# Kernel tuning notes

Hardware: AMD Instinct MI355X
Metric: run time of the kernel (lower is better)

Reference implementation:

```python
import jax, jax.numpy as jnp
import numpy as np

D_MODEL = 2048
N_HEADS = 16
D_HEAD = 128
N_GROUPS = 4          # KV heads = N_HEADS // N_GROUPS = 4
D_FF = 2048           # hard-coded default in FeedForward
EPS = 1e-6


def setup_inputs() -> dict:
    key = jax.random.key(0)
    ks = jax.random.split(key, 16)
    B, S = 4, 1024
    Hkv = N_HEADS // N_GROUPS
    s = 0.02
    inp = {
        "x": jax.random.normal(ks[0], (B, S, D_MODEL), jnp.float32),
        "scale1": jnp.ones((D_MODEL,), jnp.float32),
        "Wq": jax.random.normal(ks[1], (D_MODEL, N_HEADS * D_HEAD), jnp.float32) * s,
        "bq": jnp.zeros((N_HEADS * D_HEAD,), jnp.float32),
        "Wk": jax.random.normal(ks[2], (D_MODEL, Hkv * D_HEAD), jnp.float32) * s,
        "bk": jnp.zeros((Hkv * D_HEAD,), jnp.float32),
        "Wv": jax.random.normal(ks[3], (D_MODEL, Hkv * D_HEAD), jnp.float32) * s,
        "bv": jnp.zeros((Hkv * D_HEAD,), jnp.float32),
        "Wo": jax.random.normal(ks[4], (N_HEADS * D_HEAD, D_MODEL), jnp.float32) * s,
        "bo": jnp.zeros((D_MODEL,), jnp.float32),
        "W1": jax.random.normal(ks[5], (D_MODEL, D_FF), jnp.float32) * s,
        "b1": jnp.zeros((D_FF,), jnp.float32),
        "W2": jax.random.normal(ks[6], (D_FF, D_MODEL), jnp.float32) * s,
        "b2": jnp.zeros((D_MODEL,), jnp.float32),
    }
    return inp


def _rmsnorm(x, scale):
    rms = jnp.sqrt(jnp.mean(x * x, axis=-1, keepdims=True) + EPS)
    return scale * (x / rms)


def reference(x, scale1, Wq, bq, Wk, bk, Wv, bv, Wo, bo, W1, b1, W2, b2):
    B, S, _ = x.shape
    Hkv = N_HEADS // N_GROUPS
    xn = _rmsnorm(x, scale1)  # [B,S,D]

    # GQA attention (prefill, step=None -> no cache)
    Q = (xn @ Wq + bq).reshape(B, S, N_HEADS, D_HEAD).transpose(0, 2, 1, 3)  # [B,H,S,d]
    K = (xn @ Wk + bk).reshape(B, S, Hkv, D_HEAD).transpose(0, 2, 1, 3)      # [B,Hkv,S,d]
    V = (xn @ Wv + bv).reshape(B, S, Hkv, D_HEAD).transpose(0, 2, 1, 3)
    Kr = jnp.repeat(K, N_GROUPS, axis=1)  # [B,H,S,d]
    Vr = jnp.repeat(V, N_GROUPS, axis=1)
    scores = jnp.einsum("bhqd,bhkd->bhqk", Q, Kr) / jnp.sqrt(jnp.float32(D_HEAD))
    attn = jax.nn.softmax(scores, axis=-1)
    out = jnp.einsum("bhqk,bhkd->bhqd", attn, Vr)  # [B,H,S,d]
    out = out.transpose(0, 2, 1, 3).reshape(B, S, N_HEADS * D_HEAD)
    x = x + out @ Wo + bo

    # Source bug preserved: FFN consumes rms_norm1 output, rms_norm2 is dead code
    h = xn @ W1 + b1
    h = h * jax.nn.sigmoid(h) * h  # x_ff * silu(x_ff)
    x = x + h @ W2 + b2
    return x
```

## Files before the change

kernel.cpp:

```cpp
#include <hip/hip_runtime.h>
#include <hip/hip_bf16.h>
#include <cstdint>

using bf16 = __hip_bfloat16;
typedef __attribute__((ext_vector_type(8))) __bf16 bf16x8;
typedef __attribute__((ext_vector_type(4))) float f32x4;

#define MFMA16(a, b, c) __builtin_amdgcn_mfma_f32_16x16x32_bf16((a), (b), (c), 0, 0, 0)

#if __has_builtin(__builtin_amdgcn_exp2f)
__device__ __forceinline__ float fexp2(float x) { return __builtin_amdgcn_exp2f(x); }
#else
__device__ __forceinline__ float fexp2(float x) { return exp2f(x); }
#endif

__device__ __forceinline__ void async16(void* lds_ptr, const void* gptr) {
  auto g = reinterpret_cast<__attribute__((address_space(1))) unsigned int*>(
      reinterpret_cast<uintptr_t>(gptr));
  auto l = reinterpret_cast<__attribute__((address_space(3))) unsigned int*>(
      static_cast<unsigned int>(reinterpret_cast<uintptr_t>(lds_ptr)));
  __builtin_amdgcn_global_load_lds(g, l, 16, 0, 0);
}

__global__ __launch_bounds__(256) void rmsnorm_cast_k(
    const float* __restrict__ x, const float* __restrict__ sc, bf16* __restrict__ xn) {
  const int row = blockIdx.x, tid = threadIdx.x;
  const float4* xr = (const float4*)(x + (size_t)row * 2048);
  float4 a = xr[tid * 2], b = xr[tid * 2 + 1];
  float ss = a.x * a.x + a.y * a.y + a.z * a.z + a.w * a.w +
             b.x * b.x + b.y * b.y + b.z * b.z + b.w * b.w;
#pragma unroll
  for (int d = 1; d < 64; d <<= 1) ss += __shfl_xor(ss, d);
  __shared__ float sm[4];
  if ((tid & 63) == 0) sm[tid >> 6] = ss;
  __syncthreads();
  const float rinv = rsqrtf((sm[0] + sm[1] + sm[2] + sm[3]) * (1.0f / 2048.0f) + 1e-6f);
  const float4* sp = (const float4*)sc;
  float4 s0 = sp[tid * 2], s1 = sp[tid * 2 + 1];
  union { bf16 h[8]; bf16x8 v; } o;
  o.h[0] = __float2bfloat16(a.x * rinv * s0.x);
  o.h[1] = __float2bfloat16(a.y * rinv * s0.y);
  o.h[2] = __float2bfloat16(a.z * rinv * s0.z);
  o.h[3] = __float2bfloat16(a.w * rinv * s0.w);
  o.h[4] = __float2bfloat16(b.x * rinv * s1.x);
  o.h[5] = __float2bfloat16(b.y * rinv * s1.y);
  o.h[6] = __float2bfloat16(b.z * rinv * s1.z);
  o.h[7] = __float2bfloat16(b.w * rinv * s1.w);
  *(bf16x8*)(xn + (size_t)row * 2048 + tid * 8) = o.v;
}

__global__ void transpose_cast_k(const float* __restrict__ W, bf16* __restrict__ Wt,
                                 int N, int ldt, int row_off, int k_off) {
  __shared__ float t[32][33];
  const int n0 = blockIdx.x * 32, k0 = blockIdx.y * 32;
  const int tx = threadIdx.x, ty = threadIdx.y;
#pragma unroll
  for (int i = 0; i < 4; ++i)
    t[ty + 8 * i][tx] = W[(size_t)(k0 + ty + 8 * i) * N + n0 + tx];
  __syncthreads();
#pragma unroll
  for (int i = 0; i < 4; ++i)
    Wt[(size_t)(row_off + n0 + ty + 8 * i) * ldt + k_off + k0 + tx] =
        __float2bfloat16(t[tx][ty + 8 * i]);
}

__global__ void transpose_v_k(const bf16* __restrict__ qkv, bf16* __restrict__ vtb) {
  __shared__ bf16 t[32][33];
  const int bh = blockIdx.z, b = bh >> 2, g = bh & 3;
  const int s0 = blockIdx.x * 32, d0 = blockIdx.y * 32;
  const int tx = threadIdx.x, ty = threadIdx.y;
#pragma unroll
  for (int i = 0; i < 4; ++i)
    t[ty + 8 * i][tx] =
        qkv[(size_t)(b * 1024 + s0 + ty + 8 * i) * 3072 + 2560 + g * 128 + d0 + tx];
  __syncthreads();
#pragma unroll
  for (int i = 0; i < 4; ++i)
    vtb[((size_t)bh * 128 + d0 + ty + 8 * i) * 1024 + s0 + tx] = t[tx][ty + 8 * i];
}

__global__ void concat_bias_k(const float* __restrict__ bq, const float* __restrict__ bk,
                              const float* __restrict__ bv, const float* __restrict__ b1,
                              const float* __restrict__ bo, const float* __restrict__ b2,
                              float* __restrict__ o) {
  const int i = blockIdx.x * 256 + threadIdx.x;
  if (i < 2048) o[i] = bq[i];
  else if (i < 2560) o[i] = bk[i - 2048];
  else if (i < 3072) o[i] = bv[i - 2560];
  else if (i < 5120) o[i] = b1[i - 3072];
  else o[i] = bo[i - 5120] + b2[i - 5120];
}

#define BARRIER() \
  { asm volatile("" ::: "memory"); __builtin_amdgcn_s_barrier(); asm volatile("" ::: "memory"); }
#define LGKM0() \
  { asm volatile("s_waitcnt lgkmcnt(0)" ::: "memory"); __builtin_amdgcn_sched_barrier(0); }
#define VM_MAIN                                                          \
  { if constexpr (LPS == 4) { asm volatile("s_waitcnt vmcnt(8)" ::: "memory"); } \
    else { asm volatile("s_waitcnt vmcnt(6)" ::: "memory"); }            \
    __builtin_amdgcn_sched_barrier(0); }
#define VM_ONE                                                           \
  { if constexpr (LPS == 4) { asm volatile("s_waitcnt vmcnt(4)" ::: "memory"); } \
    else { asm volatile("s_waitcnt vmcnt(3)" ::: "memory"); }            \
    __builtin_amdgcn_sched_barrier(0); }
#define VM_ZERO \
  { asm volatile("s_waitcnt vmcnt(0)" ::: "memory"); __builtin_amdgcn_sched_barrier(0); }

#define READ_AF(MILO)                                                              \
  { unsigned char* ab_ = lds + (h_ & 3) * SLOTA;                                   \
    _Pragma("unroll") for (int i_ = 0; i_ < MI / 2; ++i_) {                        \
      const int R_ = arow0 + ((MILO) + i_) * 16;                                   \
      af[i_] = *(const bf16x8*)(ab_ + R_ * 64 + ((hi ^ ((R_ >> 1) & 3)) << 4)); } }

#define READ_BF()                                                                  \
  { unsigned char* bb_ = lds + 4 * SLOTA + (h_ & 3) * SLOTB;                       \
    _Pragma("unroll") for (int j_ = 0; j_ < NJ; ++j_) {                            \
      const int S_ = bcol0 + j_ * 16;                                              \
      bf[j_] = *(const bf16x8*)(bb_ + S_ * 64 + ((hi ^ ((S_ >> 1) & 3)) << 4)); } }

#define MFMA_HALF(MILO)                                                            \
  __builtin_amdgcn_s_setprio(1);                                                   \
  _Pragma("unroll") for (int i_ = 0; i_ < MI / 2; ++i_)                            \
    _Pragma("unroll") for (int j_ = 0; j_ < NJ; ++j_)                              \
      acc[(MILO) + i_][j_] = MFMA16(af[i_], bf[j_], acc[(MILO) + i_][j_]);         \
  __builtin_amdgcn_s_setprio(0);

#define GSLOT(H, DOSTG, VMSTMT)                                                    \
  { const int h_ = (H);                                                            \
    READ_AF(0); READ_BF();                                                         \
    if (DOSTG) stgA(h_ + 3);                                                       \
    BARRIER(); LGKM0();                                                            \
    MFMA_HALF(0);                                                                  \
    BARRIER();                                                                     \
    READ_AF(MI / 2);                                                               \
    if (DOSTG) stgB(h_ + 3);                                                       \
    VMSTMT;                                                                        \
    BARRIER(); LGKM0();                                                            \
    MFMA_HALF(MI / 2);                                                             \
    BARRIER(); }

template <int MI, int NJ, int WM, int WN, int EPI>
__global__ __launch_bounds__(512, 1) void gemm8(
    const bf16* __restrict__ A, const bf16* __restrict__ A2,
    const bf16* __restrict__ Bt, const float* __restrict__ bias,
    const float* __restrict__ res, void* __restrict__ out0,
    void* __restrict__ out1, int K) {
  constexpr int BM = WM * MI * 16;
  constexpr int BN = WN * NJ * 16;
  constexpr int SLOTA = BM * 64;
  constexpr int SLOTB = BN * 64;
  constexpr int NSWA = SLOTA / 8192;
  constexpr int NSWB = SLOTB / 8192;
  constexpr int FRACB = SLOTB % 8192;
  constexpr int LPS = NSWA + NSWB;
  extern __shared__ unsigned char lds[];

  const int tid = threadIdx.x, lane = tid & 63, w = tid >> 6;
  const int wr = w / WN, wc = w % WN;
  const int hi = lane >> 4, lo = lane & 15;

  const int lid = blockIdx.y * 16 + blockIdx.x;
  const int swz = (lid & 7) * 32 + (lid >> 3);
  const int brow = (swz & 15) * BM;
  const int bcol = (swz >> 4) * BN;

  const int NS = K >> 5;

  size_t offA[NSWA];
#pragma unroll
  for (int i = 0; i < NSWA; ++i) {
    const int o = i * 8192 + tid * 16;
    const int r = o >> 6;
    const int c = ((((o >> 4) & 3) ^ ((r >> 1) & 3)) << 3);
    offA[i] = (size_t)(brow + r) * 2048 + c;
  }
  const bf16* srcB[NSWB + (FRACB ? 1 : 0)];
#pragma unroll
  for (int i = 0; i < NSWB + (FRACB ? 1 : 0); ++i) {
    const int o = i * 8192 + tid * 16;
    const int r = o >> 6;
    const int c = ((((o >> 4) & 3) ^ ((r >> 1) & 3)) << 3);
    srcB[i] = Bt + (size_t)(bcol + r) * K + c;
  }

  auto stgA = [&](int h) {
    unsigned char* ab = lds + (h & 3) * SLOTA;
    const int kb = h * 32;
    const bf16* base;
    int ko;
    if constexpr (EPI == 1) { base = (kb < 2048) ? A : A2; ko = kb & 2047; }
    else { base = A; ko = kb; }
#pragma unroll
    for (int i = 0; i < NSWA; ++i)
      async16(ab + i * 8192 + tid * 16, base + offA[i] + ko);
  };
  auto stgB = [&](int h) {
    unsigned char* bb = lds + 4 * SLOTA + (h & 3) * SLOTB;
    const int kb = h * 32;
#pragma unroll
    for (int i = 0; i < NSWB; ++i)
      async16(bb + i * 8192 + tid * 16, srcB[i] + kb);
    if constexpr (FRACB != 0) {
      if (tid < FRACB / 16)
        async16(bb + NSWB * 8192 + tid * 16, srcB[NSWB] + kb);
    }
  };

  const int arow0 = wr * (MI * 16) + lo;
  const int bcol0 = wc * (NJ * 16) + lo;

  stgA(0); stgB(0); stgA(1); stgB(1); stgA(2); stgB(2);
  VM_MAIN;
  BARRIER();

  f32x4 acc[MI][NJ] = {};
  bf16x8 af[MI / 2], bf[NJ];

  for (int h = 0; h < NS - 3; ++h) { GSLOT(h, true, VM_MAIN); }
  GSLOT(NS - 3, false, VM_ONE);
  GSLOT(NS - 2, false, VM_ZERO);
  GSLOT(NS - 1, false, (void)0);

#pragma unroll
  for (int mi = 0; mi < MI; ++mi) {
    const int row = brow + wr * (MI * 16) + mi * 16 + hi * 4;
#pragma unroll
    for (int nj = 0; nj < NJ; ++nj) {
      const int col = bcol + wc * (NJ * 16) + nj * 16 + lo;
      const float bs = bias[col];
#pragma unroll
      for (int r = 0; r < 4; ++r) {
        float v = acc[mi][nj][r] + bs;
        if constexpr (EPI == 0) {
          if (col < 3072) {
            ((bf16*)out0)[(size_t)(row + r) * 3072 + col] = __float2bfloat16(v);
          } else {
            const float sg = 1.0f / (1.0f + __expf(-v));
            ((bf16*)out1)[(size_t)(row + r) * 2048 + (col - 3072)] =
                __float2bfloat16(v * sg * v);
          }
        } else {
          v += res[(size_t)(row + r) * 2048 + col];
          ((float*)out0)[(size_t)(row + r) * 2048 + col] = v;
        }
      }
    }
  }
}

__global__ __launch_bounds__(256, 4) void attn_fwd(
    const bf16* __restrict__ qkv, const bf16* __restrict__ vtb, bf16* __restrict__ out) {
  __shared__ __align__(16) unsigned char alds[40960];
  unsigned char* Ks = alds;
  unsigned char* Vs = alds + 16384;
  unsigned char* Ps = alds + 32768;
  const int tid = threadIdx.x, lane = tid & 63, w = tid >> 6;
  const int hi = lane >> 4, lo = lane & 15;
  const int qt = blockIdx.x, bh = blockIdx.y;
  const int b = bh >> 4, h = bh & 15, g = h >> 2;
  const size_t tok0 = (size_t)b * 1024;
  const int q0 = qt * 64;

  bf16x8 qf[4];
  {
    const bf16* qp = qkv + (tok0 + q0 + w * 16 + lo) * 3072 + h * 128 + hi * 8;
#pragma unroll
    for (int kc = 0; kc < 4; ++kc) qf[kc] = *(const bf16x8*)(qp + kc * 32);
  }

  float m2 = -1e30f, lsum = 0.f;
  f32x4 oacc[8] = {};
  const float c2 = 0.08838834764831845f * 1.44269504088896f;

  const int o = tid * 16;
  const bf16* kbase = qkv + tok0 * 3072 + 2048 + g * 128;
  const bf16* vbase = vtb + (size_t)(b * 4 + g) * 128 * 1024;
  unsigned char* Pw = Ps + w * 2048;

  for (int t = 0; t < 16; ++t) {
    const int kb = t * 64;
#pragma unroll
    for (int rd = 0; rd < 4; ++rd) {
      const int oo = o + rd * 4096;
      const int rK = oo >> 8, cK = ((oo >> 4) & 15) ^ (rK & 15);
      const int rV = oo >> 7, cV = ((oo >> 4) & 7) ^ (rV & 7);
      async16(Ks + oo, kbase + (size_t)(kb + rK) * 3072 + cK * 8);
      async16(Vs + oo, vbase + (size_t)rV * 1024 + kb + cV * 8);
    }
    __syncthreads();

    f32x4 sc[4] = {};
#pragma unroll
    for (int kc = 0; kc < 4; ++kc) {
#pragma unroll
      for (int kg = 0; kg < 4; ++kg) {
        const int row = kg * 16 + lo;
        bf16x8 kf = *(const bf16x8*)(Ks + row * 256 + ((((kc << 2) + hi) ^ (row & 15)) << 4));
        sc[kg] = MFMA16(kf, qf[kc], sc[kg]);
      }
    }

    float mx = sc[0][0];
#pragma unroll
    for (int kg = 0; kg < 4; ++kg)
#pragma unroll
      for (int r = 0; r < 4; ++r) mx = fmaxf(mx, sc[kg][r]);
    mx = fmaxf(mx, __shfl_xor(mx, 16));
    mx = fmaxf(mx, __shfl_xor(mx, 32));
    mx *= c2;
    const float mn = fmaxf(m2, mx);
    const float corr = fexp2(m2 - mn);
    m2 = mn;

    float rs = 0.f;
#pragma unroll
    for (int kg = 0; kg < 4; ++kg) {
      union { bf16 hh[4]; uint2 v; } pk;
#pragma unroll
      for (int r = 0; r < 4; ++r) {
        const float p = fexp2(sc[kg][r] * c2 - mn);
        rs += p;
        pk.hh[r] = __float2bfloat16(p);
      }
      *(uint2*)(Pw + lo * 128 + ((((kg << 1) + (hi >> 1)) ^ (lo & 7)) << 4) +
                ((hi & 1) << 3)) = pk.v;
    }
    rs += __shfl_xor(rs, 16);
    rs += __shfl_xor(rs, 32);
    lsum = lsum * corr + rs;

    float corr_r[4];
#pragma unroll
    for (int r = 0; r < 4; ++r) corr_r[r] = __shfl(corr, hi * 4 + r);
#pragma unroll
    for (int dg = 0; dg < 8; ++dg)
#pragma unroll
      for (int r = 0; r < 4; ++r) oacc[dg][r] *= corr_r[r];

    asm volatile("s_waitcnt lgkmcnt(0)" ::: "memory");

    bf16x8 pf[2];
#pragma unroll
    for (int kc = 0; kc < 2; ++kc)
      pf[kc] = *(const bf16x8*)(Pw + lo * 128 + ((((kc << 2) + hi) ^ (lo & 7)) << 4));
#pragma unroll
    for (int dg = 0; dg < 8; ++dg) {
#pragma unroll
      for (int kc = 0; kc < 2; ++kc) {
        const int vrow = dg * 16 + lo;
        bf16x8 vf = *(const bf16x8*)(Vs + vrow * 128 + ((((kc << 2) + hi) ^ (vrow & 7)) << 4));
        oacc[dg] = MFMA16(pf[kc], vf, oacc[dg]);
      }
    }
    __syncthreads();
  }

  const float linv = 1.0f / lsum;
  float lr[4];
#pragma unroll
  for (int r = 0; r < 4; ++r) lr[r] = __shfl(linv, hi * 4 + r);
  bf16* op = out + (tok0 + q0 + w * 16 + hi * 4) * 2048 + h * 128 + lo;
#pragma unroll
  for (int dg = 0; dg < 8; ++dg)
#pragma unroll
    for (int r = 0; r < 4; ++r)
      op[(size_t)r * 2048 + dg * 16] = __float2bfloat16(oacc[dg][r] * lr[r]);
}

extern "C" void kernel_launch(void* const* d_in, const int* in_sizes, int n_in,
                              void* d_out, int out_size, void* d_ws, size_t ws_size,
                              hipStream_t stream) {
  (void)in_sizes; (void)n_in; (void)out_size; (void)ws_size;
  const float* x  = (const float*)d_in[0];
  const float* s1 = (const float*)d_in[1];
  const float* Wq = (const float*)d_in[2];
  const float* bq = (const float*)d_in[3];
  const float* Wk = (const float*)d_in[4];
  const float* bk = (const float*)d_in[5];
  const float* Wv = (const float*)d_in[6];
  const float* bv = (const float*)d_in[7];
  const float* Wo = (const float*)d_in[8];
  const float* bo = (const float*)d_in[9];
  const float* W1 = (const float*)d_in[10];
  const float* b1 = (const float*)d_in[11];
  const float* W2 = (const float*)d_in[12];
  const float* b2 = (const float*)d_in[13];
  float* outp = (float*)d_out;

  char* ws = (char*)d_ws;
  bf16*  xn     = (bf16*)(ws + 0);
  bf16*  vtb    = (bf16*)(ws + 0);
  bf16*  wcatT  = (bf16*)(ws + 16777216);
  bf16*  attnb  = (bf16*)(ws + 16777216);
  float* bcat   = (float*)(ws + 37748736);
  bf16*  wcat2T = (bf16*)(ws + 37781504);
  bf16*  qkvb   = (bf16*)(ws + 54558720);
  bf16*  gbuf   = (bf16*)(ws + 79724544);

  const dim3 b32x8(32, 8);
  rmsnorm_cast_k<<<dim3(4096), dim3(256), 0, stream>>>(x, s1, xn);
  concat_bias_k<<<dim3(28), dim3(256), 0, stream>>>(bq, bk, bv, b1, bo, b2, bcat);
  transpose_cast_k<<<dim3(64, 64), b32x8, 0, stream>>>(Wq, wcatT, 2048, 2048, 0, 0);
  transpose_cast_k<<<dim3(16, 64), b32x8, 0, stream>>>(Wk, wcatT, 512, 2048, 2048, 0);
  transpose_cast_k<<<dim3(16, 64), b32x8, 0, stream>>>(Wv, wcatT, 512, 2048, 2560, 0);
  transpose_cast_k<<<dim3(64, 64), b32x8, 0, stream>>>(W1, wcatT, 2048, 2048, 3072, 0);
  transpose_cast_k<<<dim3(64, 64), b32x8, 0, stream>>>(Wo, wcat2T, 2048, 4096, 0, 0);
  transpose_cast_k<<<dim3(64, 64), b32x8, 0, stream>>>(W2, wcat2T, 2048, 4096, 0, 2048);
  gemm8<8, 5, 2, 4, 0><<<dim3(16, 16), dim3(512), 147456, stream>>>(
      xn, xn, wcatT, bcat, (const float*)nullptr, (void*)qkvb, (void*)gbuf, 2048);
  transpose_v_k<<<dim3(32, 4, 16), b32x8, 0, stream>>>(qkvb, vtb);
  attn_fwd<<<dim3(16, 64), dim3(256), 0, stream>>>(qkvb, vtb, attnb);
  gemm8<4, 4, 4, 2, 1><<<dim3(16, 16), dim3(512), 98304, stream>>>(
      attnb, gbuf, wcat2T, bcat + 5120, x, (void*)outp, (void*)nullptr, 4096);
}
```

Baseline: 262.0 us.

## Split-K the output GEMM into bf16 partials with a separate reduce kernel

The second GEMM (attention-out plus FFN-down, K=4096) now launches over two K-halves along blockIdx.z. It uses larger 256x256 tiles, so each block covers 16 rows of output tiles with half the K loop, and each half writes bf16 partials. A new reduce kernel adds x, both partials and the combined bias into the fp32 output. The first GEMM is regenerated with 640 threads (5 warp columns), and both GEMMs declare launch bounds for 2 blocks per CU. This trades an extra memory pass and bf16 rounding of the partials for shorter per-block K loops and different tile and occupancy characteristics.

```diff
diff --git a/kernel.cpp b/kernel.cpp
--- a/kernel.cpp
+++ b/kernel.cpp
@@ -13,6 +13,11 @@
 #else
 __device__ __forceinline__ float fexp2(float x) { return exp2f(x); }
 #endif
+
+template <int N>
+__device__ __forceinline__ void vmwait() {
+  asm volatile("s_waitcnt vmcnt(%0)" ::"i"(N) : "memory");
+}
 
 __device__ __forceinline__ void async16(void* lds_ptr, const void* gptr) {
   auto g = reinterpret_cast<__attribute__((address_space(1))) unsigned int*>(
@@ -95,156 +100,172 @@
   { asm volatile("" ::: "memory"); __builtin_amdgcn_s_barrier(); asm volatile("" ::: "memory"); }
 #define LGKM0() \
   { asm volatile("s_waitcnt lgkmcnt(0)" ::: "memory"); __builtin_amdgcn_sched_barrier(0); }
-#define VM_MAIN                                                          \
-  { if constexpr (LPS == 4) { asm volatile("s_waitcnt vmcnt(8)" ::: "memory"); } \
-    else { asm volatile("s_waitcnt vmcnt(6)" ::: "memory"); }            \
+#define VMW_PAIR(NH, NL)                                                     \
+  { if constexpr (REMA) {                                                    \
+      if (w < REMA / 64) vmwait<NH>(); else vmwait<NL>();                    \
+    } else { vmwait<NL>(); }                                                 \
     __builtin_amdgcn_sched_barrier(0); }
-#define VM_ONE                                                           \
-  { if constexpr (LPS == 4) { asm volatile("s_waitcnt vmcnt(4)" ::: "memory"); } \
-    else { asm volatile("s_waitcnt vmcnt(3)" ::: "memory"); }            \
-    __builtin_amdgcn_sched_barrier(0); }
-#define VM_ZERO \
-  { asm volatile("s_waitcnt vmcnt(0)" ::: "memory"); __builtin_amdgcn_sched_barrier(0); }
-
-#define READ_AF(MILO)                                                              \
-  { unsigned char* ab_ = lds + (h_ & 3) * SLOTA;                                   \
-    _Pragma("unroll") for (int i_ = 0; i_ < MI / 2; ++i_) {                        \
-      const int R_ = arow0 + ((MILO) + i_) * 16;                                   \
+
+#define RD_A(MILO)                                                                 \
+  { unsigned char* ab_ = lds + sl_ * SLOTA;                                        \
+    _Pragma("unroll") for (int i_ = 0; i_ < 4; ++i_) {                             \
+      const int R_ = wr * 128 + ((MILO) + i_) * 16 + lo;                           \
       af[i_] = *(const bf16x8*)(ab_ + R_ * 64 + ((hi ^ ((R_ >> 1) & 3)) << 4)); } }
 
-#define READ_BF()                                                                  \
-  { unsigned char* bb_ = lds + 4 * SLOTA + (h_ & 3) * SLOTB;                       \
-    _Pragma("unroll") for (int j_ = 0; j_ < NJ; ++j_) {                            \
-      const int S_ = bcol0 + j_ * 16;                                              \
+#define RD_B()                                                                     \
+  { unsigned char* bb_ = lds + 4 * SLOTA + sl_ * SLOTB;                            \
+    _Pragma("unroll") for (int j_ = 0; j_ < 4; ++j_) {                             \
+      const int S_ = wc * 64 + j_ * 16 + lo;                                       \
       bf[j_] = *(const bf16x8*)(bb_ + S_ * 64 + ((hi ^ ((S_ >> 1) & 3)) << 4)); } }
 
-#define MFMA_HALF(MILO)                                                            \
+#define MM(MILO)                                                                   \
   __builtin_amdgcn_s_setprio(1);                                                   \
-  _Pragma("unroll") for (int i_ = 0; i_ < MI / 2; ++i_)                            \
-    _Pragma("unroll") for (int j_ = 0; j_ < NJ; ++j_)                              \
+  _Pragma("unroll") for (int i_ = 0; i_ < 4; ++i_)                                 \
+    _Pragma("unroll") for (int j_ = 0; j_ < 4; ++j_)                               \
       acc[(MILO) + i_][j_] = MFMA16(af[i_], bf[j_], acc[(MILO) + i_][j_]);         \
   __builtin_amdgcn_s_setprio(0);
 
-#define GSLOT(H, DOSTG, VMSTMT)                                                    \
-  { const int h_ = (H);                                                            \
-    READ_AF(0); READ_BF();                                                         \
+#define DO_SLOT(H, DOSTG, VMSTMT)                                                  \
+  { const int h_ = (H); const int sl_ = h_ & 3;                                    \
+    RD_A(0); RD_B();                                                               \
     if (DOSTG) stgA(h_ + 3);                                                       \
     BARRIER(); LGKM0();                                                            \
-    MFMA_HALF(0);                                                                  \
+    MM(0);                                                                         \
     BARRIER();                                                                     \
-    READ_AF(MI / 2);                                                               \
+    RD_A(4);                                                                       \
     if (DOSTG) stgB(h_ + 3);                                                       \
     VMSTMT;                                                                        \
     BARRIER(); LGKM0();                                                            \
-    MFMA_HALF(MI / 2);                                                             \
+    MM(4);                                                                         \
     BARRIER(); }
 
-template <int MI, int NJ, int WM, int WN, int EPI>
-__global__ __launch_bounds__(512, 1) void gemm8(
+template <int WN, int EPI>
+__global__ __launch_bounds__(WN * 128, 2) void gemm8(
     const bf16* __restrict__ A, const bf16* __restrict__ A2,
     const bf16* __restrict__ Bt, const float* __restrict__ bias,
-    const float* __restrict__ res, void* __restrict__ out0,
-    void* __restrict__ out1, int K) {
-  constexpr int BM = WM * MI * 16;
-  constexpr int BN = WN * NJ * 16;
+    void* __restrict__ out0, void* __restrict__ out1, int ldB) {
+  constexpr int T = WN * 128;
+  constexpr int BM = 256;
+  constexpr int BN = WN * 64;
   constexpr int SLOTA = BM * 64;
   constexpr int SLOTB = BN * 64;
-  constexpr int NSWA = SLOTA / 8192;
-  constexpr int NSWB = SLOTB / 8192;
-  constexpr int FRACB = SLOTB % 8192;
-  constexpr int LPS = NSWA + NSWB;
+  constexpr int SWEEP = T * 16;
+  constexpr int FULLA = SLOTA / SWEEP, REMA = (SLOTA % SWEEP) / 16;
+  constexpr int FULLB = SLOTB / SWEEP, REMB = (SLOTB % SWEEP) / 16;
+  static_assert(REMB == 0 && (REMA % 64) == 0, "sweep alignment");
+  constexpr int LL = FULLA + FULLB, LH = LL + (REMA ? 1 : 0);
   extern __shared__ unsigned char lds[];
 
   const int tid = threadIdx.x, lane = tid & 63, w = tid >> 6;
   const int wr = w / WN, wc = w % WN;
   const int hi = lane >> 4, lo = lane & 15;
 
-  const int lid = blockIdx.y * 16 + blockIdx.x;
+  const int lid = (blockIdx.z * gridDim.y + blockIdx.y) * gridDim.x + blockIdx.x;
   const int swz = (lid & 7) * 32 + (lid >> 3);
   const int brow = (swz & 15) * BM;
-  const int bcol = (swz >> 4) * BN;
-
-  const int NS = K >> 5;
-
-  size_t offA[NSWA];
-#pragma unroll
-  for (int i = 0; i < NSWA; ++i) {
-    const int o = i * 8192 + tid * 16;
-    const int r = o >> 6;
-    const int c = ((((o >> 4) & 3) ^ ((r >> 1) & 3)) << 3);
-    offA[i] = (size_t)(brow + r) * 2048 + c;
-  }
-  const bf16* srcB[NSWB + (FRACB ? 1 : 0)];
-#pragma unroll
-  for (int i = 0; i < NSWB + (FRACB ? 1 : 0); ++i) {
-    const int o = i * 8192 + tid * 16;
-    const int r = o >> 6;
-    const int c = ((((o >> 4) & 3) ^ ((r >> 1) & 3)) << 3);
-    srcB[i] = Bt + (size_t)(bcol + r) * K + c;
+  int bcol, z;
+  if constexpr (EPI == 1) {
+    const int r = swz >> 4;
+    bcol = (r & 7) * BN;
+    z = r >> 3;
+  } else {
+    bcol = (swz >> 4) * BN;
+    z = 0;
+  }
+  const bf16* Ab = (EPI == 1 && z) ? A2 : A;
+  const int koff = (EPI == 1) ? z * 2048 : 0;
+
+  const int NS = 64;
+
+  const bf16* Asrc[FULLA + (REMA ? 1 : 0)];
+#pragma unroll
+  for (int i = 0; i < FULLA + (REMA ? 1 : 0); ++i) {
+    const int o = i * SWEEP + tid * 16;
+    const int r = o >> 6, c = ((o >> 4) & 3) ^ ((r >> 1) & 3);
+    Asrc[i] = Ab + (size_t)(brow + r) * 2048 + c * 8;
+  }
+  const bf16* Bsrc[FULLB];
+#pragma unroll
+  for (int i = 0; i < FULLB; ++i) {
+    const int o = i * SWEEP + tid * 16;
+    const int r = o >> 6, c = ((o >> 4) & 3) ^ ((r >> 1) & 3);
+    Bsrc[i] = Bt + (size_t)(bcol + r) * ldB + koff + c * 8;
   }
 
   auto stgA = [&](int h) {
     unsigned char* ab = lds + (h & 3) * SLOTA;
     const int kb = h * 32;
-    const bf16* base;
-    int ko;
-    if constexpr (EPI == 1) { base = (kb < 2048) ? A : A2; ko = kb & 2047; }
-    else { base = A; ko = kb; }
-#pragma unroll
-    for (int i = 0; i < NSWA; ++i)
-      async16(ab + i * 8192 + tid * 16, base + offA[i] + ko);
+#pragma unroll
+    for (int i = 0; i < FULLA; ++i)
+      async16(ab + i * SWEEP + tid * 16, Asrc[i] + kb);
+    if constexpr (REMA != 0) {
+      if (tid < REMA)
+        async16(ab + FULLA * SWEEP + tid * 16, Asrc[FULLA] + kb);
+    }
   };
   auto stgB = [&](int h) {
     unsigned char* bb = lds + 4 * SLOTA + (h & 3) * SLOTB;
     const int kb = h * 32;
 #pragma unroll
-    for (int i = 0; i < NSWB; ++i)
-      async16(bb + i * 8192 + tid * 16, srcB[i] + kb);
-    if constexpr (FRACB != 0) {
-      if (tid < FRACB / 16)
-        async16(bb + NSWB * 8192 + tid * 16, srcB[NSWB] + kb);
-    }
+    for (int i = 0; i < FULLB; ++i)
+      async16(bb + i * SWEEP + tid * 16, Bsrc[i] + kb);
   };
 
-  const int arow0 = wr * (MI * 16) + lo;
-  const int bcol0 = wc * (NJ * 16) + lo;
-
   stgA(0); stgB(0); stgA(1); stgB(1); stgA(2); stgB(2);
-  VM_MAIN;
+  VMW_PAIR(2 * LH, 2 * LL);
   BARRIER();
 
-  f32x4 acc[MI][NJ] = {};
-  bf16x8 af[MI / 2], bf[NJ];
-
-  for (int h = 0; h < NS - 3; ++h) { GSLOT(h, true, VM_MAIN); }
-  GSLOT(NS - 3, false, VM_ONE);
-  GSLOT(NS - 2, false, VM_ZERO);
-  GSLOT(NS - 1, false, (void)0);
-
-#pragma unroll
-  for (int mi = 0; mi < MI; ++mi) {
-    const int row = brow + wr * (MI * 16) + mi * 16 + hi * 4;
-#pragma unroll
-    for (int nj = 0; nj < NJ; ++nj) {
-      const int col = bcol + wc * (NJ * 16) + nj * 16 + lo;
-      const float bs = bias[col];
+  f32x4 acc[8][4] = {};
+  bf16x8 af[4], bf[4];
+
+  for (int h = 0; h < NS - 3; ++h) { DO_SLOT(h, true, VMW_PAIR(2 * LH, 2 * LL)); }
+  DO_SLOT(NS - 3, false, VMW_PAIR(LH, LL));
+  DO_SLOT(NS - 2, false, VMW_PAIR(0, 0));
+  DO_SLOT(NS - 1, false, (void)0);
+
+#pragma unroll
+  for (int mi = 0; mi < 8; ++mi) {
+    const int row0 = brow + wr * 128 + mi * 16 + hi * 4;
+#pragma unroll
+    for (int nj = 0; nj < 4; ++nj) {
+      const int col = bcol + wc * 64 + nj * 16 + lo;
 #pragma unroll
       for (int r = 0; r < 4; ++r) {
-        float v = acc[mi][nj][r] + bs;
+        const int row = row0 + r;
         if constexpr (EPI == 0) {
+          float v = acc[mi][nj][r] + bias[col];
           if (col < 3072) {
-            ((bf16*)out0)[(size_t)(row + r) * 3072 + col] = __float2bfloat16(v);
+            ((bf16*)out0)[(size_t)row * 3072 + col] = __float2bfloat16(v);
           } else {
             const float sg = 1.0f / (1.0f + __expf(-v));
-            ((bf16*)out1)[(size_t)(row + r) * 2048 + (col - 3072)] =
+            ((bf16*)out1)[(size_t)row * 2048 + (col - 3072)] =
                 __float2bfloat16(v * sg * v);
           }
         } else {
-          v += res[(size_t)(row + r) * 2048 + col];
-          ((float*)out0)[(size_t)(row + r) * 2048 + col] = v;
+          bf16* P = (bf16*)(z ? out1 : out0);
+          P[(size_t)row * 2048 + col] = __float2bfloat16(acc[mi][nj][r]);
         }
       }
     }
+  }
+}
+
+__global__ __launch_bounds__(256) void reduce_k(
+    const float* __restrict__ x, const bf16* __restrict__ P0,
+    const bf16* __restrict__ P1, const float* __restrict__ bias,
+    float* __restrict__ out) {
+  const int n4 = 4096 * 2048 / 4;
+  for (int i = blockIdx.x * 256 + threadIdx.x; i < n4; i += gridDim.x * 256) {
+    float4 xv = ((const float4*)x)[i];
+    ushort4 a = ((const ushort4*)P0)[i];
+    ushort4 b = ((const ushort4*)P1)[i];
+    float4 bv = ((const float4*)bias)[i & 511];
+    float4 o;
+    o.x = xv.x + __uint_as_float((unsigned)a.x << 16) + __uint_as_float((unsigned)b.x << 16) + bv.x;
+    o.y = xv.y + __uint_as_float((unsigned)a.y << 16) + __uint_as_float((unsigned)b.y << 16) + bv.y;
+    o.z = xv.z + __uint_as_float((unsigned)a.z << 16) + __uint_as_float((unsigned)b.z << 16) + bv.z;
+    o.w = xv.w + __uint_as_float((unsigned)a.w << 16) + __uint_as_float((unsigned)b.w << 16) + bv.w;
+    ((float4*)out)[i] = o;
   }
 }
 
@@ -390,11 +411,13 @@
   char* ws = (char*)d_ws;
   bf16*  xn     = (bf16*)(ws + 0);
   bf16*  vtb    = (bf16*)(ws + 0);
+  bf16*  P0     = (bf16*)(ws + 0);
   bf16*  wcatT  = (bf16*)(ws + 16777216);
   bf16*  attnb  = (bf16*)(ws + 16777216);
   float* bcat   = (float*)(ws + 37748736);
   bf16*  wcat2T = (bf16*)(ws + 37781504);
   bf16*  qkvb   = (bf16*)(ws + 54558720);
+  bf16*  P1     = (bf16*)(ws + 54558720);
   bf16*  gbuf   = (bf16*)(ws + 79724544);
 
   const dim3 b32x8(32, 8);
@@ -406,10 +429,11 @@
   transpose_cast_k<<<dim3(64, 64), b32x8, 0, stream>>>(W1, wcatT, 2048, 2048, 3072, 0);
   transpose_cast_k<<<dim3(64, 64), b32x8, 0, stream>>>(Wo, wcat2T, 2048, 4096, 0, 0);
   transpose_cast_k<<<dim3(64, 64), b32x8, 0, stream>>>(W2, wcat2T, 2048, 4096, 0, 2048);
-  gemm8<8, 5, 2, 4, 0><<<dim3(16, 16), dim3(512), 147456, stream>>>(
-      xn, xn, wcatT, bcat, (const float*)nullptr, (void*)qkvb, (void*)gbuf, 2048);
+  gemm8<5, 0><<<dim3(16, 16), dim3(640), 147456, stream>>>(
+      xn, (const bf16*)nullptr, wcatT, bcat, (void*)qkvb, (void*)gbuf, 2048);
   transpose_v_k<<<dim3(32, 4, 16), b32x8, 0, stream>>>(qkvb, vtb);
   attn_fwd<<<dim3(16, 64), dim3(256), 0, stream>>>(qkvb, vtb, attnb);
-  gemm8<4, 4, 4, 2, 1><<<dim3(16, 16), dim3(512), 98304, stream>>>(
-      attnb, gbuf, wcat2T, bcat + 5120, x, (void*)outp, (void*)nullptr, 4096);
-}
+  gemm8<4, 1><<<dim3(16, 8, 2), dim3(512), 131072, stream>>>(
+      attnb, gbuf, wcat2T, (const float*)nullptr, (void*)P0, (void*)P1, 4096);
+  reduce_k<<<dim3(2048), dim3(256), 0, stream>>>(x, P0, P1, bcat + 5120, outp);
+}
```

Result: slower. 303.7 us (+15.9%).
